# Kernel optimization log

Hardware: AMD Instinct MI355X
Metric: run time of the kernel (lower is better)

The kernel has to match this reference:

```python
import math
import jax, jax.numpy as jnp
import numpy as np

N_HEADS = 16
D_EMBED = 1024
D_HEAD = D_EMBED // N_HEADS  # 64; only used for the scale factor (see bug note)
B, N = 4, 4096


def setup_inputs() -> dict:
    key = jax.random.key(0)
    k1, k2, k3, k4, k5 = jax.random.split(key, 5)
    return {
        "x": jax.random.normal(k1, (B, N, D_EMBED), dtype=jnp.float32),
        "W_qkv_w": jax.random.normal(k2, (3 * D_EMBED, D_EMBED), dtype=jnp.float32) * 0.02,
        "W_qkv_b": jax.random.normal(k3, (3 * D_EMBED,), dtype=jnp.float32) * 0.02,
        "W_o_w": jax.random.normal(k4, (D_EMBED, D_EMBED), dtype=jnp.float32) * 0.02,
        "W_o_b": jax.random.normal(k5, (D_EMBED,), dtype=jnp.float32) * 0.02,
    }


def reference(x, W_qkv_w, W_qkv_b, W_o_w, W_o_b):
    # Faithful to source, including its bugs:
    #  - q/k/v are never actually reshaped to heads (the .view().transpose()
    #    results are discarded), so attention runs over full d_embed vectors
    #    with scale 1/sqrt(d_head).
    #  - the final transpose(1,2).reshape scrambles the output layout.
    b, n, d = x.shape
    qkv = x @ W_qkv_w.T + W_qkv_b                      # [b, n, 3d]
    q, k, v = jnp.split(qkv, 3, axis=-1)               # each [b, n, d]
    scores = jnp.einsum("bqd,bkd->bqk", q, k)          # [b, n, n]
    causal = jnp.triu(jnp.ones((n, n), dtype=bool), 1)
    scale = jnp.float32(1.0 / math.sqrt(D_HEAD))
    scores = jnp.where(causal, -jnp.inf, scores * scale)
    weights = jax.nn.softmax(scores, axis=-1)
    out = jnp.einsum("bqk,bkd->bqd", weights, v)       # [b, n, d]
    out = jnp.swapaxes(out, 1, 2).reshape(b, n, d)     # scramble (as in source)
    return out @ W_o_w.T + W_o_b
```

## Files before the change

### kernel.cpp

```cpp
#include <hip/hip_runtime.h>
#include <math.h>

#define TB 256

typedef __attribute__((ext_vector_type(8))) short short8_t;
typedef __attribute__((ext_vector_type(4))) float f32x4;

__device__ __forceinline__ ushort f2bf(float f) {
    uint u = __float_as_uint(f);
    return (ushort)((u + 0x7FFFu + ((u >> 16) & 1u)) >> 16);
}

__device__ __forceinline__ void gload_lds16(const void* g, void* l) {
    __builtin_amdgcn_global_load_lds(
        (const __attribute__((address_space(1))) void*)g,
        (__attribute__((address_space(3))) void*)l, 16, 0, 0);
}

template<int CONV, int EPI, bool TRI, bool KLIM>
__global__ __launch_bounds__(TB)
void gemm_bf16(const void* __restrict__ Av, int lda,
               const ushort* __restrict__ B, int ldb,
               const float* __restrict__ bias,
               void* __restrict__ Cv, int ldc,
               int M, int Nc, int K, float alpha, int off)
{
    constexpr int BM = 128, BN = 128, BK = 32;
    const int m0 = blockIdx.y * BM;
    const int n0 = blockIdx.x * BN;
    if (TRI && n0 > m0 + off + BM - 1) return;

    const int tid = threadIdx.x;
    const int lane = tid & 63;
    const int wid = tid >> 6;
    const int wr = wid >> 1, wc = wid & 1;

    __shared__ __align__(16) ushort As[2][BM * BK];
    __shared__ __align__(16) ushort Bs[2][BN * BK];

    f32x4 acc[4][4];
    const f32x4 zero = {0.f, 0.f, 0.f, 0.f};
    #pragma unroll
    for (int mi = 0; mi < 4; mi++)
        #pragma unroll
        for (int ni = 0; ni < 4; ni++) acc[mi][ni] = zero;

    const int klim = KLIM ? (n0 + off + BN) : K;
    const int kend = klim < K ? klim : K;
    const int nt = kend / BK;

    auto STAGE = [&](int t, int bufi) {
        const int k0 = t * BK;
        if (CONV) {
            const float* Af = (const float*)Av;
            #pragma unroll
            for (int h = 0; h < 2; h++) {
                const int q = tid + h * TB;
                const int row = q >> 2;
                const int kp = (q & 3) * 8;
                const float* src = &Af[(size_t)(m0 + row) * lda + k0 + kp];
                float4 u0 = *(const float4*)src;
                float4 u1 = *(const float4*)(src + 4);
                short8_t s;
                s[0] = (short)f2bf(u0.x); s[1] = (short)f2bf(u0.y);
                s[2] = (short)f2bf(u0.z); s[3] = (short)f2bf(u0.w);
                s[4] = (short)f2bf(u1.x); s[5] = (short)f2bf(u1.y);
                s[6] = (short)f2bf(u1.z); s[7] = (short)f2bf(u1.w);
                *(short8_t*)&As[bufi][row * BK + kp] = s;
            }
        } else {
            const ushort* Ab = (const ushort*)Av;
            #pragma unroll
            for (int h = 0; h < 2; h++) {
                const int c = wid * 2 + h;
                const int row = c * 16 + (lane >> 2);
                const int kh  = (lane & 3) * 8;
                gload_lds16(&Ab[(size_t)(m0 + row) * lda + k0 + kh],
                            (char*)&As[bufi][0] + c * 1024);
            }
        }
        #pragma unroll
        for (int h = 0; h < 2; h++) {
            const int c = wid * 2 + h;
            const int row = c * 16 + (lane >> 2);
            const int kh  = (lane & 3) * 8;
            gload_lds16(&B[(size_t)(n0 + row) * ldb + k0 + kh],
                        (char*)&Bs[bufi][0] + c * 1024);
        }
    };

    STAGE(0, 0);
    __syncthreads();

    for (int t = 0; t < nt; t++) {
        const int cur = t & 1;
        if (t + 1 < nt) STAGE(t + 1, cur ^ 1);

        const int frow = lane & 15;
        const int kh8  = (lane >> 4) * 8;
        short8_t a[4], b[4];
        #pragma unroll
        for (int mi = 0; mi < 4; mi++)
            a[mi] = *(const short8_t*)&As[cur][(wr * 64 + mi * 16 + frow) * BK + kh8];
        #pragma unroll
        for (int ni = 0; ni < 4; ni++)
            b[ni] = *(const short8_t*)&Bs[cur][(wc * 64 + ni * 16 + frow) * BK + kh8];
        #pragma unroll
        for (int mi = 0; mi < 4; mi++)
            #pragma unroll
            for (int ni = 0; ni < 4; ni++)
                acc[mi][ni] = __builtin_amdgcn_mfma_f32_16x16x32_bf16(
                    a[mi], b[ni], acc[mi][ni], 0, 0, 0);
        __syncthreads();
    }

    const int col = lane & 15;
    const int rb  = (lane >> 4) * 4;
    #pragma unroll
    for (int mi = 0; mi < 4; mi++) {
        #pragma unroll
        for (int ni = 0; ni < 4; ni++) {
            const int r = m0 + wr * 64 + mi * 16 + rb;
            const int c = n0 + wc * 64 + ni * 16 + col;
            f32x4 v = acc[mi][ni];
            if (EPI == 0) {
                ushort* C = (ushort*)Cv;
                const float bz = bias[c];
                #pragma unroll
                for (int t = 0; t < 4; t++)
                    C[(size_t)(r + t) * ldc + c] = f2bf(v[t] + bz);
            } else if (EPI == 1) {
                float* C = (float*)Cv;
                #pragma unroll
                for (int t = 0; t < 4; t++)
                    C[(size_t)(r + t) * ldc + c] = v[t] * alpha;
            } else if (EPI == 2) {
                ushort* C = (ushort*)Cv;
                #pragma unroll
                for (int t = 0; t < 4; t++)
                    C[(size_t)(r + t) * ldc + c + off] = f2bf(v[t]);
            } else {
                float* C = (float*)Cv;
                const float bz = bias[c];
                #pragma unroll
                for (int t = 0; t < 4; t++)
                    C[(size_t)(r + t) * ldc + c] = v[t] + bz;
            }
        }
    }
}

__global__ __launch_bounds__(TB)
void conv_f32_bf16(const float* __restrict__ in, ushort* __restrict__ out, int n4)
{
    for (int i = blockIdx.x * TB + threadIdx.x; i < n4; i += gridDim.x * TB) {
        float4 v = ((const float4*)in)[i];
        ushort4 o;
        o.x = f2bf(v.x); o.y = f2bf(v.y); o.z = f2bf(v.z); o.w = f2bf(v.w);
        ((ushort4*)out)[i] = o;
    }
}

__global__ __launch_bounds__(TB)
void transposeV(const ushort* __restrict__ V, int ldv, ushort* __restrict__ Vt)
{
    __shared__ ushort Ls[64][65];
    const int n0 = blockIdx.x * 64, d0 = blockIdx.y * 64;
    const int t = threadIdx.x;
    #pragma unroll
    for (int p = 0; p < 4; p++) {
        const int row = p * 16 + (t >> 4);
        const int c4 = (t & 15) * 4;
        ushort4 v = *(const ushort4*)&V[(size_t)(n0 + row) * ldv + d0 + c4];
        Ls[row][c4 + 0] = v.x; Ls[row][c4 + 1] = v.y;
        Ls[row][c4 + 2] = v.z; Ls[row][c4 + 3] = v.w;
    }
    __syncthreads();
    #pragma unroll
    for (int p = 0; p < 4; p++) {
        const int d = p * 16 + (t >> 4);
        const int n4 = (t & 15) * 4;
        ushort4 o;
        o.x = Ls[n4 + 0][d]; o.y = Ls[n4 + 1][d];
        o.z = Ls[n4 + 2][d]; o.w = Ls[n4 + 3][d];
        *(ushort4*)&Vt[(size_t)(d0 + d) * 4096 + n0 + n4] = o;
    }
}

__global__ __launch_bounds__(TB)
void softmax_prefix(float* __restrict__ S, ushort* __restrict__ P, int r0)
{
    const int local = blockIdx.x;
    const int r = r0 + local;
    const int pe = ((r >> 7) << 7) + 128;
    float* p = S + (size_t)local * 4096;
    ushort* q = P + (size_t)local * 4096;
    const int t = threadIdx.x;
    const int wv = t >> 6, ln = t & 63;
    __shared__ float red[4];

    float lm = -INFINITY;
    for (int k4 = t * 4; k4 < pe; k4 += 1024) {
        float4 v = *(const float4*)&p[k4];
        lm = (k4 + 0 <= r) ? fmaxf(lm, v.x) : lm;
        lm = (k4 + 1 <= r) ? fmaxf(lm, v.y) : lm;
        lm = (k4 + 2 <= r) ? fmaxf(lm, v.z) : lm;
        lm = (k4 + 3 <= r) ? fmaxf(lm, v.w) : lm;
    }
    #pragma unroll
    for (int m = 1; m < 64; m <<= 1) lm = fmaxf(lm, __shfl_xor(lm, m, 64));
    if (ln == 0) red[wv] = lm;
    __syncthreads();
    const float mx = fmaxf(fmaxf(red[0], red[1]), fmaxf(red[2], red[3]));
    __syncthreads();

    float ls = 0.f;
    for (int k4 = t * 4; k4 < pe; k4 += 1024) {
        float4 v = *(const float4*)&p[k4];
        float4 e;
        e.x = (k4 + 0 <= r) ? __expf(v.x - mx) : 0.f;
        e.y = (k4 + 1 <= r) ? __expf(v.y - mx) : 0.f;
        e.z = (k4 + 2 <= r) ? __expf(v.z - mx) : 0.f;
        e.w = (k4 + 3 <= r) ? __expf(v.w - mx) : 0.f;
        ls += e.x + e.y + e.z + e.w;
        *(float4*)&p[k4] = e;
    }
    #pragma unroll
    for (int m = 1; m < 64; m <<= 1) ls += __shfl_xor(ls, m, 64);
    if (ln == 0) red[wv] = ls;
    __syncthreads();
    const float inv = 1.0f / (red[0] + red[1] + red[2] + red[3]);
    for (int k4 = t * 4; k4 < pe; k4 += 1024) {
        float4 e = *(const float4*)&p[k4];
        ushort4 o;
        o.x = f2bf(e.x * inv); o.y = f2bf(e.y * inv);
        o.z = f2bf(e.z * inv); o.w = f2bf(e.w * inv);
        *(ushort4*)&q[k4] = o;
    }
}

extern "C" void kernel_launch(void* const* d_in, const int* in_sizes, int n_in,
                              void* d_out, int out_size, void* d_ws, size_t ws_size,
                              hipStream_t stream)
{
    const float* x    = (const float*)d_in[0];
    const float* Wqkv = (const float*)d_in[1];
    const float* bqkv = (const float*)d_in[2];
    const float* Wo   = (const float*)d_in[3];
    const float* bo   = (const float*)d_in[4];
    float* out = (float*)d_out;

    ushort* Wq   = (ushort*)d_ws;
    ushort* Wob  = Wq   + (size_t)3072 * 1024;
    ushort* qkvb = Wob  + (size_t)1024 * 1024;
    ushort* Vtb  = qkvb + (size_t)4096 * 3072;
    ushort* Tall = Vtb  + (size_t)1024 * 4096;
    ushort* Pch  = Tall + (size_t)4 * 4096 * 1024;
    const size_t fixedB = ((size_t)3072 * 1024 + (size_t)1024 * 1024 +
                           (size_t)4096 * 3072 + (size_t)1024 * 4096 +
                           (size_t)4 * 4096 * 1024) * 2;
    int CH = 4096;
    while (CH > 512 && fixedB + (size_t)CH * 4096 * 6 > ws_size) CH >>= 1;
    float* Sch = (float*)(Pch + (size_t)CH * 4096);

    dim3 blk(TB);

    conv_f32_bf16<<<256, blk, 0, stream>>>(Wqkv, Wq,  3072 * 1024 / 4);
    conv_f32_bf16<<<128, blk, 0, stream>>>(Wo,   Wob, 1024 * 1024 / 4);

    for (int b = 0; b < 4; b++) {
        const float* xb = x + (size_t)b * 4096 * 1024;
        gemm_bf16<1, 0, false, false><<<dim3(24, 32), blk, 0, stream>>>(
            xb, 1024, Wq, 1024, bqkv, qkvb, 3072, 4096, 3072, 1024, 1.f, 0);

        transposeV<<<dim3(64, 16), blk, 0, stream>>>(qkvb + 2048, 3072, Vtb);

        const ushort* Qb = qkvb;
        const ushort* Kb = qkvb + 1024;

        for (int r0 = 0; r0 < 4096; r0 += CH) {
            gemm_bf16<0, 1, true, false><<<dim3(32, CH / 128), blk, 0, stream>>>(
                Qb + (size_t)r0 * 3072, 3072, Kb, 3072, nullptr,
                Sch, 4096, CH, 4096, 1024, 0.125f, r0);
            softmax_prefix<<<dim3(CH), blk, 0, stream>>>(Sch, Pch, r0);
            gemm_bf16<0, 2, false, true><<<dim3(CH / 128, 8), blk, 0, stream>>>(
                Vtb, 4096, Pch, 4096, nullptr,
                Tall + (size_t)b * 4096 * 1024, 4096, 1024, CH, 4096, 1.f, r0);
        }
    }

    gemm_bf16<0, 3, false, false><<<dim3(8, 128), blk, 0, stream>>>(
        Tall, 1024, Wob, 1024, bo, out, 1024, 16384, 1024, 1024, 1.f, 0);
}
```

Baseline: 838.6 us.

## Batch all four sequences into single launches via grid z-dimension

Adds a batched path that processes all four batch elements in each GEMM, transpose and softmax launch using blockIdx.z strides, instead of looping per batch. It also reverses the block order in the P·V GEMM so the causally longer blocks are scheduled first. The aim is fewer kernel launches and fuller GPU occupancy on the triangular stages. This needs a much larger workspace, and when the workspace is too small the code falls back to the old per-batch loop.

New measurement: 959.2 us. +14.4%, slower.

```diff
diff --git a/kernel.cpp b/kernel.cpp
--- a/kernel.cpp
+++ b/kernel.cpp
@@ -17,18 +17,24 @@
         (__attribute__((address_space(3))) void*)l, 16, 0, 0);
 }
 
-template<int CONV, int EPI, bool TRI, bool KLIM>
+template<int CONV, int EPI, bool TRI, bool KLIM, bool REVX>
 __global__ __launch_bounds__(TB)
 void gemm_bf16(const void* __restrict__ Av, int lda,
-               const ushort* __restrict__ B, int ldb,
+               const ushort* __restrict__ Bp, int ldb,
                const float* __restrict__ bias,
                void* __restrict__ Cv, int ldc,
-               int M, int Nc, int K, float alpha, int off)
+               int K, float alpha, int off,
+               size_t strA, size_t strB, size_t strC)
 {
     constexpr int BM = 128, BN = 128, BK = 32;
     const int m0 = blockIdx.y * BM;
-    const int n0 = blockIdx.x * BN;
+    const int nb = REVX ? (gridDim.x - 1 - blockIdx.x) : blockIdx.x;
+    const int n0 = nb * BN;
     if (TRI && n0 > m0 + off + BM - 1) return;
+
+    const void*   Az = (const char*)Av + (size_t)blockIdx.z * strA;
+    const ushort* B  = (const ushort*)((const char*)Bp + (size_t)blockIdx.z * strB);
+    void*         Cz = (char*)Cv + (size_t)blockIdx.z * strC;
 
     const int tid = threadIdx.x;
     const int lane = tid & 63;
@@ -52,7 +58,7 @@
     auto STAGE = [&](int t, int bufi) {
         const int k0 = t * BK;
         if (CONV) {
-            const float* Af = (const float*)Av;
+            const float* Af = (const float*)Az;
             #pragma unroll
             for (int h = 0; h < 2; h++) {
                 const int q = tid + h * TB;
@@ -69,7 +75,7 @@
                 *(short8_t*)&As[bufi][row * BK + kp] = s;
             }
         } else {
-            const ushort* Ab = (const ushort*)Av;
+            const ushort* Ab = (const ushort*)Az;
             #pragma unroll
             for (int h = 0; h < 2; h++) {
                 const int c = wid * 2 + h;
@@ -124,23 +130,23 @@
             const int c = n0 + wc * 64 + ni * 16 + col;
             f32x4 v = acc[mi][ni];
             if (EPI == 0) {
-                ushort* C = (ushort*)Cv;
+                ushort* C = (ushort*)Cz;
                 const float bz = bias[c];
                 #pragma unroll
                 for (int t = 0; t < 4; t++)
                     C[(size_t)(r + t) * ldc + c] = f2bf(v[t] + bz);
             } else if (EPI == 1) {
-                float* C = (float*)Cv;
+                float* C = (float*)Cz;
                 #pragma unroll
                 for (int t = 0; t < 4; t++)
                     C[(size_t)(r + t) * ldc + c] = v[t] * alpha;
             } else if (EPI == 2) {
-                ushort* C = (ushort*)Cv;
+                ushort* C = (ushort*)Cz;
                 #pragma unroll
                 for (int t = 0; t < 4; t++)
                     C[(size_t)(r + t) * ldc + c + off] = f2bf(v[t]);
             } else {
-                float* C = (float*)Cv;
+                float* C = (float*)Cz;
                 const float bz = bias[c];
                 #pragma unroll
                 for (int t = 0; t < 4; t++)
@@ -162,8 +168,11 @@
 }
 
 __global__ __launch_bounds__(TB)
-void transposeV(const ushort* __restrict__ V, int ldv, ushort* __restrict__ Vt)
-{
+void transposeV(const ushort* __restrict__ Vp, int ldv, ushort* __restrict__ Vtp,
+                size_t strV, size_t strVt)
+{
+    const ushort* V = (const ushort*)((const char*)Vp + (size_t)blockIdx.z * strV);
+    ushort* Vt = (ushort*)((char*)Vtp + (size_t)blockIdx.z * strVt);
     __shared__ ushort Ls[64][65];
     const int n0 = blockIdx.x * 64, d0 = blockIdx.y * 64;
     const int t = threadIdx.x;
@@ -188,13 +197,14 @@
 }
 
 __global__ __launch_bounds__(TB)
-void softmax_prefix(float* __restrict__ S, ushort* __restrict__ P, int r0)
+void softmax_prefix(float* __restrict__ Sp, ushort* __restrict__ Pp, int r0)
 {
     const int local = blockIdx.x;
     const int r = r0 + local;
     const int pe = ((r >> 7) << 7) + 128;
-    float* p = S + (size_t)local * 4096;
-    ushort* q = P + (size_t)local * 4096;
+    const size_t rowoff = ((size_t)blockIdx.y * gridDim.x + local) * 4096;
+    float* p = Sp + rowoff;
+    ushort* q = Pp + rowoff;
     const int t = threadIdx.x;
     const int wv = t >> 6, ln = t & 63;
     __shared__ float red[4];
@@ -250,45 +260,81 @@
     const float* bo   = (const float*)d_in[4];
     float* out = (float*)d_out;
 
+    dim3 blk(TB);
+    const size_t B_QKV = (size_t)4096 * 3072;
+    const size_t B_VT  = (size_t)1024 * 4096;
+
+    const size_t fixedA = ((size_t)3072 * 1024 + (size_t)1024 * 1024 +
+                           4 * B_QKV + 4 * B_VT + 4 * B_VT) * 2;
+    int CHa = 4096;
+    while (CHa > 512 && fixedA + (size_t)4 * CHa * 4096 * 6 > ws_size) CHa >>= 1;
+
+    if (fixedA + (size_t)4 * CHa * 4096 * 6 <= ws_size) {
+        ushort* Wq   = (ushort*)d_ws;
+        ushort* Wob  = Wq   + (size_t)3072 * 1024;
+        ushort* qkvA = Wob  + (size_t)1024 * 1024;
+        ushort* VtA  = qkvA + 4 * B_QKV;
+        ushort* TA   = VtA  + 4 * B_VT;
+        ushort* Pch  = TA   + 4 * B_VT;
+        float*  Sch  = (float*)(Pch + (size_t)4 * CHa * 4096);
+
+        conv_f32_bf16<<<256, blk, 0, stream>>>(Wqkv, Wq,  3072 * 1024 / 4);
+        conv_f32_bf16<<<128, blk, 0, stream>>>(Wo,   Wob, 1024 * 1024 / 4);
+
+        gemm_bf16<1, 0, false, false, false><<<dim3(24, 128), blk, 0, stream>>>(
+            x, 1024, Wq, 1024, bqkv, qkvA, 3072, 1024, 1.f, 0, 0, 0, 0);
+
+        transposeV<<<dim3(64, 16, 4), blk, 0, stream>>>(
+            qkvA + 2048, 3072, VtA, B_QKV * 2, B_VT * 2);
+
+        for (int r0 = 0; r0 < 4096; r0 += CHa) {
+            gemm_bf16<0, 1, true, false, false><<<dim3(32, CHa / 128, 4), blk, 0, stream>>>(
+                qkvA + (size_t)r0 * 3072, 3072, qkvA + 1024, 3072, nullptr,
+                Sch, 4096, 1024, 0.125f, r0,
+                B_QKV * 2, B_QKV * 2, (size_t)CHa * 4096 * 4);
+            softmax_prefix<<<dim3(CHa, 4), blk, 0, stream>>>(Sch, Pch, r0);
+            gemm_bf16<0, 2, false, true, true><<<dim3(CHa / 128, 8, 4), blk, 0, stream>>>(
+                VtA, 4096, Pch, 4096, nullptr, TA, 4096, 4096, 1.f, r0,
+                B_VT * 2, (size_t)CHa * 4096 * 2, B_VT * 2);
+        }
+
+        gemm_bf16<0, 3, false, false, false><<<dim3(8, 128), blk, 0, stream>>>(
+            TA, 1024, Wob, 1024, bo, out, 1024, 1024, 1.f, 0, 0, 0, 0);
+        return;
+    }
+
     ushort* Wq   = (ushort*)d_ws;
     ushort* Wob  = Wq   + (size_t)3072 * 1024;
     ushort* qkvb = Wob  + (size_t)1024 * 1024;
-    ushort* Vtb  = qkvb + (size_t)4096 * 3072;
-    ushort* Tall = Vtb  + (size_t)1024 * 4096;
+    ushort* Vtb  = qkvb + B_QKV;
+    ushort* Tall = Vtb  + B_VT;
     ushort* Pch  = Tall + (size_t)4 * 4096 * 1024;
     const size_t fixedB = ((size_t)3072 * 1024 + (size_t)1024 * 1024 +
-                           (size_t)4096 * 3072 + (size_t)1024 * 4096 +
-                           (size_t)4 * 4096 * 1024) * 2;
+                           B_QKV + B_VT + (size_t)4 * 4096 * 1024) * 2;
     int CH = 4096;
-    while (CH > 512 && fixedB + (size_t)CH * 4096 * 6 > ws_size) CH >>= 1;
+    while (CH > 128 && fixedB + (size_t)CH * 4096 * 6 > ws_size) CH >>= 1;
     float* Sch = (float*)(Pch + (size_t)CH * 4096);
-
-    dim3 blk(TB);
 
     conv_f32_bf16<<<256, blk, 0, stream>>>(Wqkv, Wq,  3072 * 1024 / 4);
     conv_f32_bf16<<<128, blk, 0, stream>>>(Wo,   Wob, 1024 * 1024 / 4);
 
     for (int b = 0; b < 4; b++) {
         const float* xb = x + (size_t)b * 4096 * 1024;
-        gemm_bf16<1, 0, false, false><<<dim3(24, 32), blk, 0, stream>>>(
-            xb, 1024, Wq, 1024, bqkv, qkvb, 3072, 4096, 3072, 1024, 1.f, 0);
-
-        transposeV<<<dim3(64, 16), blk, 0, stream>>>(qkvb + 2048, 3072, Vtb);
-
-        const ushort* Qb = qkvb;
-        const ushort* Kb = qkvb + 1024;
+        gemm_bf16<1, 0, false, false, false><<<dim3(24, 32), blk, 0, stream>>>(
+            xb, 1024, Wq, 1024, bqkv, qkvb, 3072, 1024, 1.f, 0, 0, 0, 0);
+        transposeV<<<dim3(64, 16), blk, 0, stream>>>(qkvb + 2048, 3072, Vtb, 0, 0);
 
         for (int r0 = 0; r0 < 4096; r0 += CH) {
-            gemm_bf16<0, 1, true, false><<<dim3(32, CH / 128), blk, 0, stream>>>(
-                Qb + (size_t)r0 * 3072, 3072, Kb, 3072, nullptr,
-                Sch, 4096, CH, 4096, 1024, 0.125f, r0);
-            softmax_prefix<<<dim3(CH), blk, 0, stream>>>(Sch, Pch, r0);
-            gemm_bf16<0, 2, false, true><<<dim3(CH / 128, 8), blk, 0, stream>>>(
+            gemm_bf16<0, 1, true, false, false><<<dim3(32, CH / 128), blk, 0, stream>>>(
+                qkvb + (size_t)r0 * 3072, 3072, qkvb + 1024, 3072, nullptr,
+                Sch, 4096, 1024, 0.125f, r0, 0, 0, 0);
+            softmax_prefix<<<dim3(CH, 1), blk, 0, stream>>>(Sch, Pch, r0);
+            gemm_bf16<0, 2, false, true, true><<<dim3(CH / 128, 8), blk, 0, stream>>>(
                 Vtb, 4096, Pch, 4096, nullptr,
-                Tall + (size_t)b * 4096 * 1024, 4096, 1024, CH, 4096, 1.f, r0);
-        }
-    }
-
-    gemm_bf16<0, 3, false, false><<<dim3(8, 128), blk, 0, stream>>>(
-        Tall, 1024, Wob, 1024, bo, out, 1024, 16384, 1024, 1024, 1.f, 0);
-}
+                Tall + (size_t)b * 4096 * 1024, 4096, 4096, 1.f, r0, 0, 0, 0);
+        }
+    }
+
+    gemm_bf16<0, 3, false, false, false><<<dim3(8, 128), blk, 0, stream>>>(
+        Tall, 1024, Wob, 1024, bo, out, 1024, 1024, 1.f, 0, 0, 0, 0);
+}
```

## Triple-buffer GEMM LDS pipeline, pre-convert x to bf16, reverse PV block order

Applied to the files above, without the earlier changes.

The GEMM now keeps three LDS stages and prefetches two tiles ahead, waiting with explicit vmcnt counts and a bare s_barrier instead of a full __syncthreads per iteration. The in-kernel fp32-to-bf16 conversion of x in the QKV projection is removed; x is converted once up front by a separate kernel so every GEMM uses the async global-to-LDS path. The P·V GEMM walks its column blocks in reverse so the longest causal K-ranges are scheduled first, improving load balance. The cost is more LDS per block, which may lower occupancy, and an extra pass over x.

New measurement: 860.1 us. 1.03x slower.

```diff
diff --git a/kernel.cpp b/kernel.cpp
--- a/kernel.cpp
+++ b/kernel.cpp
@@ -17,17 +17,18 @@
         (__attribute__((address_space(3))) void*)l, 16, 0, 0);
 }
 
-template<int CONV, int EPI, bool TRI, bool KLIM>
-__global__ __launch_bounds__(TB)
-void gemm_bf16(const void* __restrict__ Av, int lda,
+template<int EPI, bool TRI, bool KLIM, bool REVX>
+__global__ __launch_bounds__(TB)
+void gemm_bf16(const ushort* __restrict__ A, int lda,
                const ushort* __restrict__ B, int ldb,
                const float* __restrict__ bias,
                void* __restrict__ Cv, int ldc,
-               int M, int Nc, int K, float alpha, int off)
+               int K, float alpha, int off)
 {
     constexpr int BM = 128, BN = 128, BK = 32;
     const int m0 = blockIdx.y * BM;
-    const int n0 = blockIdx.x * BN;
+    const int nb = REVX ? (gridDim.x - 1 - blockIdx.x) : blockIdx.x;
+    const int n0 = nb * BN;
     if (TRI && n0 > m0 + off + BM - 1) return;
 
     const int tid = threadIdx.x;
@@ -35,8 +36,8 @@
     const int wid = tid >> 6;
     const int wr = wid >> 1, wc = wid & 1;
 
-    __shared__ __align__(16) ushort As[2][BM * BK];
-    __shared__ __align__(16) ushort Bs[2][BN * BK];
+    __shared__ __align__(16) ushort As[3][BM * BK];
+    __shared__ __align__(16) ushort Bs[3][BN * BK];
 
     f32x4 acc[4][4];
     const f32x4 zero = {0.f, 0.f, 0.f, 0.f};
@@ -49,52 +50,30 @@
     const int kend = klim < K ? klim : K;
     const int nt = kend / BK;
 
-    auto STAGE = [&](int t, int bufi) {
+    auto STAGE = [&](int t, int s) {
         const int k0 = t * BK;
-        if (CONV) {
-            const float* Af = (const float*)Av;
-            #pragma unroll
-            for (int h = 0; h < 2; h++) {
-                const int q = tid + h * TB;
-                const int row = q >> 2;
-                const int kp = (q & 3) * 8;
-                const float* src = &Af[(size_t)(m0 + row) * lda + k0 + kp];
-                float4 u0 = *(const float4*)src;
-                float4 u1 = *(const float4*)(src + 4);
-                short8_t s;
-                s[0] = (short)f2bf(u0.x); s[1] = (short)f2bf(u0.y);
-                s[2] = (short)f2bf(u0.z); s[3] = (short)f2bf(u0.w);
-                s[4] = (short)f2bf(u1.x); s[5] = (short)f2bf(u1.y);
-                s[6] = (short)f2bf(u1.z); s[7] = (short)f2bf(u1.w);
-                *(short8_t*)&As[bufi][row * BK + kp] = s;
-            }
-        } else {
-            const ushort* Ab = (const ushort*)Av;
-            #pragma unroll
-            for (int h = 0; h < 2; h++) {
-                const int c = wid * 2 + h;
-                const int row = c * 16 + (lane >> 2);
-                const int kh  = (lane & 3) * 8;
-                gload_lds16(&Ab[(size_t)(m0 + row) * lda + k0 + kh],
-                            (char*)&As[bufi][0] + c * 1024);
-            }
-        }
-        #pragma unroll
-        for (int h = 0; h < 2; h++) {
-            const int c = wid * 2 + h;
-            const int row = c * 16 + (lane >> 2);
-            const int kh  = (lane & 3) * 8;
-            gload_lds16(&B[(size_t)(n0 + row) * ldb + k0 + kh],
-                        (char*)&Bs[bufi][0] + c * 1024);
-        }
+        const int c = wid * 2;
+        const int row0 = c * 16 + (lane >> 2);
+        const int row1 = row0 + 16;
+        const int kh = (lane & 3) * 8;
+        gload_lds16(&A[(size_t)(m0 + row0) * lda + k0 + kh], (char*)&As[s][0] + c * 1024);
+        gload_lds16(&A[(size_t)(m0 + row1) * lda + k0 + kh], (char*)&As[s][0] + (c + 1) * 1024);
+        gload_lds16(&B[(size_t)(n0 + row0) * ldb + k0 + kh], (char*)&Bs[s][0] + c * 1024);
+        gload_lds16(&B[(size_t)(n0 + row1) * ldb + k0 + kh], (char*)&Bs[s][0] + (c + 1) * 1024);
     };
 
     STAGE(0, 0);
-    __syncthreads();
+    if (nt > 1) {
+        STAGE(1, 1);
+        asm volatile("s_waitcnt vmcnt(4)" ::: "memory");
+    } else {
+        asm volatile("s_waitcnt vmcnt(0)" ::: "memory");
+    }
+    __builtin_amdgcn_s_barrier();
 
     for (int t = 0; t < nt; t++) {
-        const int cur = t & 1;
-        if (t + 1 < nt) STAGE(t + 1, cur ^ 1);
+        const int cur = t % 3;
+        if (t + 2 < nt) STAGE(t + 2, (t + 2) % 3);
 
         const int frow = lane & 15;
         const int kh8  = (lane >> 4) * 8;
@@ -111,7 +90,12 @@
             for (int ni = 0; ni < 4; ni++)
                 acc[mi][ni] = __builtin_amdgcn_mfma_f32_16x16x32_bf16(
                     a[mi], b[ni], acc[mi][ni], 0, 0, 0);
-        __syncthreads();
+
+        if (t + 1 < nt) {
+            if (t + 2 < nt) asm volatile("s_waitcnt vmcnt(4)" ::: "memory");
+            else            asm volatile("s_waitcnt vmcnt(0)" ::: "memory");
+            __builtin_amdgcn_s_barrier();
+        }
     }
 
     const int col = lane & 15;
@@ -188,13 +172,13 @@
 }
 
 __global__ __launch_bounds__(TB)
-void softmax_prefix(float* __restrict__ S, ushort* __restrict__ P, int r0)
+void softmax_prefix(float* __restrict__ Sp, ushort* __restrict__ Pp, int r0)
 {
     const int local = blockIdx.x;
     const int r = r0 + local;
     const int pe = ((r >> 7) << 7) + 128;
-    float* p = S + (size_t)local * 4096;
-    ushort* q = P + (size_t)local * 4096;
+    float* p = Sp + (size_t)local * 4096;
+    ushort* q = Pp + (size_t)local * 4096;
     const int t = threadIdx.x;
     const int wv = t >> 6, ln = t & 63;
     __shared__ float red[4];
@@ -250,45 +234,44 @@
     const float* bo   = (const float*)d_in[4];
     float* out = (float*)d_out;
 
-    ushort* Wq   = (ushort*)d_ws;
+    ushort* xbf  = (ushort*)d_ws;
+    ushort* Wq   = xbf  + (size_t)4 * 4096 * 1024;
     ushort* Wob  = Wq   + (size_t)3072 * 1024;
     ushort* qkvb = Wob  + (size_t)1024 * 1024;
     ushort* Vtb  = qkvb + (size_t)4096 * 3072;
     ushort* Tall = Vtb  + (size_t)1024 * 4096;
     ushort* Pch  = Tall + (size_t)4 * 4096 * 1024;
-    const size_t fixedB = ((size_t)3072 * 1024 + (size_t)1024 * 1024 +
-                           (size_t)4096 * 3072 + (size_t)1024 * 4096 +
-                           (size_t)4 * 4096 * 1024) * 2;
+    const size_t fixedB = ((size_t)4 * 4096 * 1024 + (size_t)3072 * 1024 +
+                           (size_t)1024 * 1024 + (size_t)4096 * 3072 +
+                           (size_t)1024 * 4096 + (size_t)4 * 4096 * 1024) * 2;
     int CH = 4096;
-    while (CH > 512 && fixedB + (size_t)CH * 4096 * 6 > ws_size) CH >>= 1;
+    while (CH > 128 && fixedB + (size_t)CH * 4096 * 6 > ws_size) CH >>= 1;
     float* Sch = (float*)(Pch + (size_t)CH * 4096);
 
     dim3 blk(TB);
 
-    conv_f32_bf16<<<256, blk, 0, stream>>>(Wqkv, Wq,  3072 * 1024 / 4);
-    conv_f32_bf16<<<128, blk, 0, stream>>>(Wo,   Wob, 1024 * 1024 / 4);
+    conv_f32_bf16<<<2048, blk, 0, stream>>>(x,    xbf, 4 * 4096 * 1024 / 4);
+    conv_f32_bf16<<<256,  blk, 0, stream>>>(Wqkv, Wq,  3072 * 1024 / 4);
+    conv_f32_bf16<<<128,  blk, 0, stream>>>(Wo,   Wob, 1024 * 1024 / 4);
 
     for (int b = 0; b < 4; b++) {
-        const float* xb = x + (size_t)b * 4096 * 1024;
-        gemm_bf16<1, 0, false, false><<<dim3(24, 32), blk, 0, stream>>>(
-            xb, 1024, Wq, 1024, bqkv, qkvb, 3072, 4096, 3072, 1024, 1.f, 0);
+        const ushort* xb = xbf + (size_t)b * 4096 * 1024;
+        gemm_bf16<0, false, false, false><<<dim3(24, 32), blk, 0, stream>>>(
+            xb, 1024, Wq, 1024, bqkv, qkvb, 3072, 1024, 1.f, 0);
 
         transposeV<<<dim3(64, 16), blk, 0, stream>>>(qkvb + 2048, 3072, Vtb);
 
-        const ushort* Qb = qkvb;
-        const ushort* Kb = qkvb + 1024;
-
         for (int r0 = 0; r0 < 4096; r0 += CH) {
-            gemm_bf16<0, 1, true, false><<<dim3(32, CH / 128), blk, 0, stream>>>(
-                Qb + (size_t)r0 * 3072, 3072, Kb, 3072, nullptr,
-                Sch, 4096, CH, 4096, 1024, 0.125f, r0);
+            gemm_bf16<1, true, false, false><<<dim3(32, CH / 128), blk, 0, stream>>>(
+                qkvb + (size_t)r0 * 3072, 3072, qkvb + 1024, 3072, nullptr,
+                Sch, 4096, 1024, 0.125f, r0);
             softmax_prefix<<<dim3(CH), blk, 0, stream>>>(Sch, Pch, r0);
-            gemm_bf16<0, 2, false, true><<<dim3(CH / 128, 8), blk, 0, stream>>>(
+            gemm_bf16<2, false, true, true><<<dim3(CH / 128, 8), blk, 0, stream>>>(
                 Vtb, 4096, Pch, 4096, nullptr,
-                Tall + (size_t)b * 4096 * 1024, 4096, 1024, CH, 4096, 1.f, r0);
+                Tall + (size_t)b * 4096 * 1024, 4096, 4096, 1.f, r0);
         }
     }
 
-    gemm_bf16<0, 3, false, false><<<dim3(8, 128), blk, 0, stream>>>(
-        Tall, 1024, Wob, 1024, bo, out, 1024, 16384, 1024, 1024, 1.f, 0);
-}
+    gemm_bf16<3, false, false, false><<<dim3(8, 128), blk, 0, stream>>>(
+        Tall, 1024, Wob, 1024, bo, out, 1024, 1024, 1.f, 0);
+}
```
